# Optimization experiments

Hardware: AMD Instinct MI355X
Metric: run time of the kernel (lower is better)

## Reference

```python
import jax, jax.numpy as jnp
import numpy as np

B, D, H, E, C = 16384, 1024, 2048, 4, 3
EPS = 1e-5


def setup_inputs() -> dict:
    key = jax.random.key(0)
    ks = jax.random.split(key, 12)
    s = lambda k, shape, fan: jax.random.normal(k, shape, jnp.float32) * (1.0 / np.sqrt(fan))
    return {
        "x": jax.random.normal(ks[0], (B, D), jnp.float32),
        # gate: LayerNorm(D) -> Linear(D, E)
        "gate_ln_g": jnp.ones((D,), jnp.float32),
        "gate_ln_b": jnp.zeros((D,), jnp.float32),
        "gate_w": s(ks[1], (D, E), D),
        "gate_b": jnp.zeros((E,), jnp.float32),
        # experts (stacked over E): LayerNorm(D) -> Linear(D,H) -> GELU -> Linear(H,C)
        "ex_ln_g": jnp.ones((E, D), jnp.float32),
        "ex_ln_b": jnp.zeros((E, D), jnp.float32),
        "ex_w1": s(ks[2], (E, D, H), D),
        "ex_b1": jnp.zeros((E, H), jnp.float32),
        "ex_w2": s(ks[3], (E, H, C), H),
        "ex_b2": jnp.zeros((E, C), jnp.float32),
    }


def _normalize(x):
    # shared (x - mean) / sqrt(var + eps); per-expert affine applied separately
    mu = jnp.mean(x, axis=-1, keepdims=True)
    var = jnp.mean(jnp.square(x - mu), axis=-1, keepdims=True)
    return (x - mu) * jax.lax.rsqrt(var + EPS)


def reference(x, gate_ln_g, gate_ln_b, gate_w, gate_b,
              ex_ln_g, ex_ln_b, ex_w1, ex_b1, ex_w2, ex_b2):
    normed = _normalize(x)                              # [B, D]
    # gate: LN -> Linear -> softmax over experts
    gate_logits = (normed * gate_ln_g + gate_ln_b) @ gate_w + gate_b   # [B, E]
    gate_weights = jax.nn.softmax(gate_logits, axis=-1)               # [B, E]
    # experts (dropout inactive in eval): per-expert LN affine, MLP with exact GELU
    xn = normed[None, :, :] * ex_ln_g[:, None, :] + ex_ln_b[:, None, :]  # [E, B, D]
    h = jax.nn.gelu(jnp.einsum('ebd,edh->ebh', xn, ex_w1) + ex_b1[:, None, :],
                    approximate=False)                                   # [E, B, H]
    logits = jnp.einsum('ebh,ehc->ebc', h, ex_w2) + ex_b2[:, None, :]    # [E, B, C]
    # gated sum over experts
    return jnp.einsum('be,ebc->bc', gate_weights, logits)               # [B, C]
```

## Files before the change

kernel.cpp:

```cpp
#include <hip/hip_runtime.h>
#include <hip/hip_bf16.h>

typedef __bf16 bf16x8 __attribute__((ext_vector_type(8)));
typedef float  f32x4  __attribute__((ext_vector_type(4)));

__device__ __forceinline__ unsigned short f2bf(float f) {
    union { float f; unsigned int u; } v; v.f = f;
    unsigned int u = v.u;
    unsigned int r = (u + 0x7fffu + ((u >> 16) & 1u)) >> 16;
    return (unsigned short)r;
}

typedef const __attribute__((address_space(1))) unsigned int* gptr_t;
typedef __attribute__((address_space(3))) unsigned int* lptr_t;
__device__ __forceinline__ void async_ld16(const void* g, void* l) {
    __builtin_amdgcn_global_load_lds((gptr_t)g, (lptr_t)l, 16, 0, 0);
}

__device__ __forceinline__ float gelu_fast(float x) {
    const float c1 = 2.30223608f;
    const float c2 = 0.102944903f;
    float s  = x * x;
    float zn = x * __builtin_fmaf(s, -c2, -c1);
    float u  = __builtin_amdgcn_exp2f(zn);
    return x * __builtin_amdgcn_rcpf(1.0f + u);
}

#define Bn 16384
#define Dd 1024
#define Hh 2048
#define Ee 4
#define Cc 3

__global__ __launch_bounds__(256) void prep_and_norm(
        const float* __restrict__ x,
        const float* __restrict__ gg, const float* __restrict__ gb,
        const float* __restrict__ gw, const float* __restrict__ gbias,
        const float* __restrict__ w1, const float* __restrict__ exlng,
        const float* __restrict__ exlnb,
        unsigned short* __restrict__ normed, float* __restrict__ gate,
        unsigned short* __restrict__ w1t, float* __restrict__ b1part) {
    __shared__ float tile[64][65];
    __shared__ float red[4][64];
    const int bid = blockIdx.x, t = threadIdx.x;

    if (bid < 4096) {
        const int row  = bid * 4 + (t >> 6);
        const int lane = t & 63;
        const float4* xp = (const float4*)(x + (size_t)row * Dd);
        float4 v[4];
        float s = 0.f, q = 0.f;
        #pragma unroll
        for (int j = 0; j < 4; ++j) {
            v[j] = xp[j * 64 + lane];
            s += v[j].x + v[j].y + v[j].z + v[j].w;
            q += v[j].x * v[j].x + v[j].y * v[j].y + v[j].z * v[j].z + v[j].w * v[j].w;
        }
        #pragma unroll
        for (int off = 32; off; off >>= 1) { s += __shfl_xor(s, off); q += __shfl_xor(q, off); }
        const float mu = s * (1.f / Dd);
        const float var = q * (1.f / Dd) - mu * mu;
        const float rstd = rsqrtf(var + 1e-5f);
        float l0 = 0.f, l1 = 0.f, l2 = 0.f, l3 = 0.f;
        #pragma unroll
        for (int j = 0; j < 4; ++j) {
            const int d = j * 256 + lane * 4;
            float n[4] = { (v[j].x - mu) * rstd, (v[j].y - mu) * rstd,
                           (v[j].z - mu) * rstd, (v[j].w - mu) * rstd };
            ushort4 u; u.x = f2bf(n[0]); u.y = f2bf(n[1]); u.z = f2bf(n[2]); u.w = f2bf(n[3]);
            ((ushort4*)(normed + (size_t)row * Dd))[j * 64 + lane] = u;
            float4 g4 = ((const float4*)gg)[j * 64 + lane];
            float4 b4 = ((const float4*)gb)[j * 64 + lane];
            float a[4] = { n[0] * g4.x + b4.x, n[1] * g4.y + b4.y,
                           n[2] * g4.z + b4.z, n[3] * g4.w + b4.w };
            #pragma unroll
            for (int c = 0; c < 4; ++c) {
                float4 wv = ((const float4*)gw)[d + c];
                l0 += a[c] * wv.x; l1 += a[c] * wv.y; l2 += a[c] * wv.z; l3 += a[c] * wv.w;
            }
        }
        #pragma unroll
        for (int off = 32; off; off >>= 1) {
            l0 += __shfl_xor(l0, off); l1 += __shfl_xor(l1, off);
            l2 += __shfl_xor(l2, off); l3 += __shfl_xor(l3, off);
        }
        if (lane == 0) {
            float L0 = l0 + gbias[0], L1 = l1 + gbias[1], L2 = l2 + gbias[2], L3 = l3 + gbias[3];
            float mx = fmaxf(fmaxf(L0, L1), fmaxf(L2, L3));
            float e0 = expf(L0 - mx), e1 = expf(L1 - mx), e2 = expf(L2 - mx), e3 = expf(L3 - mx);
            float inv = 1.f / (e0 + e1 + e2 + e3);
            float4 gv; gv.x = e0 * inv; gv.y = e1 * inv; gv.z = e2 * inv; gv.w = e3 * inv;
            ((float4*)gate)[row] = gv;
        }
    } else {
        const int b2i = bid - 4096;
        const int d0b = b2i & 15, h0b = (b2i >> 4) & 31, e = b2i >> 9;
        const int d0 = d0b * 64, h0 = h0b * 64;
        const float* gp = exlng + e * Dd + d0;
        const float* lb = exlnb + e * Dd + d0;
        const float* wp = w1 + ((size_t)e * Dd + d0) * Hh + h0;
        #pragma unroll
        for (int j = 0; j < 16; ++j) {
            int idx = t + j * 256; int dl = idx >> 6, hl = idx & 63;
            tile[dl][hl] = wp[(size_t)dl * Hh + hl];
        }
        __syncthreads();
        #pragma unroll
        for (int j = 0; j < 8; ++j) {
            int idx = t + j * 256; int hl = idx >> 5, k2 = (idx & 31) * 2;
            ushort2 o; o.x = f2bf(tile[k2][hl] * gp[k2]); o.y = f2bf(tile[k2 + 1][hl] * gp[k2 + 1]);
            *(ushort2*)(w1t + ((size_t)(e * Hh + h0 + hl)) * Dd + d0 + k2) = o;
        }
        const int hl = t & 63, dq = t >> 6;
        float acc = 0.f;
        #pragma unroll
        for (int i = 0; i < 16; ++i)
            acc += lb[dq * 16 + i] * tile[dq * 16 + i][hl];
        red[dq][hl] = acc;
        __syncthreads();
        if (t < 64)
            b1part[(size_t)(e * 16 + d0b) * Hh + h0 + t] = red[0][t] + red[1][t] + red[2][t] + red[3][t];
    }
}

__global__ __launch_bounds__(512, 2) void gemm_fused(
    const unsigned short* __restrict__ A,
    const unsigned short* __restrict__ Bt,
    const float* __restrict__ b1,
    const float* __restrict__ b1part,
    const float* __restrict__ w2,
    float* __restrict__ part)
{
    __shared__ unsigned short As[4][256 * 32];
    __shared__ unsigned short Bs[4][256 * 32];
    __shared__ float w2s[256 * 3];
    __shared__ float b1s[256];

    const int L = blockIdx.x;
    const int xcd = L & 7, j = L >> 3;
    const int mb = (j >> 7) * 32 + xcd * 4 + (j & 3);
    const int nb = (j >> 2) & 31;
    const int m0 = mb * 256;
    const int n0 = nb * 256;

    const int t = threadIdx.x, lane = t & 63, wid = t >> 6;
    const int wm = wid >> 2, wn = wid & 3;
    const int quad = lane >> 4, l15 = lane & 15;

    if (t < 256) {
        const int e = n0 >> 11, hh = n0 & 2047;
        float s = b1[n0 + t];
        #pragma unroll
        for (int i = 0; i < 16; ++i)
            s += b1part[(size_t)(e * 16 + i) * Hh + hh + t];
        b1s[t] = s;
        w2s[t * 3 + 0] = w2[(n0 + t) * 3 + 0];
        w2s[t * 3 + 1] = w2[(n0 + t) * 3 + 1];
        w2s[t * 3 + 2] = w2[(n0 + t) * 3 + 2];
    }

    const int srow  = t >> 2;
    const int sslot = (t & 3) ^ ((t >> 3) & 3);
    const unsigned short* ga = A  + (size_t)(m0 + srow) * Dd + sslot * 8;
    const unsigned short* gb = Bt + (size_t)(n0 + srow) * Dd + sslot * 8;
    const int ldoff = t * 8;

#define STAGE_A(kt) { unsigned short* d = &As[(kt) & 3][ldoff];                 \
    async_ld16(ga + (kt) * 32,            d);                                   \
    async_ld16(ga + (kt) * 32 + 128 * Dd, d + 4096); }
#define STAGE_B(kt) { unsigned short* d = &Bs[(kt) & 3][ldoff];                 \
    async_ld16(gb + (kt) * 32,            d);                                   \
    async_ld16(gb + (kt) * 32 + 128 * Dd, d + 4096); }

    f32x4 acc[8][4] = {};

    const int rsw   = (l15 >> 1) & 3;
    const int aBase = (wm * 128 + l15) * 32 + ((quad ^ rsw) * 8);
    const int bBase = (wn * 64  + l15) * 32 + ((quad ^ rsw) * 8);

    STAGE_A(0); STAGE_B(0);
    STAGE_A(1); STAGE_B(1);
    __syncthreads();

    for (int kt = 0; kt < 32; ++kt) {
        const unsigned short* as = &As[kt & 3][0];
        const unsigned short* bs = &Bs[kt & 3][0];

        bf16x8 bf[4], af[8];
        #pragma unroll
        for (int ni = 0; ni < 4; ++ni) bf[ni] = *(const bf16x8*)(bs + bBase + ni * 512);
        #pragma unroll
        for (int mi = 0; mi < 8; ++mi) af[mi] = *(const bf16x8*)(as + aBase + mi * 512);

        if (kt < 30) { STAGE_A(kt + 2); STAGE_B(kt + 2); }

        if (kt < 30) {
            __asm__ volatile("s_waitcnt vmcnt(4)" ::: "memory");
        } else {
            __asm__ volatile("s_waitcnt vmcnt(0)" ::: "memory");
        }
        __builtin_amdgcn_s_barrier();
        __builtin_amdgcn_sched_barrier(0xF);

        __builtin_amdgcn_s_setprio(1);
        #pragma unroll
        for (int mi = 0; mi < 8; ++mi)
            #pragma unroll
            for (int ni = 0; ni < 4; ++ni)
                acc[mi][ni] = __builtin_amdgcn_mfma_f32_16x16x32_bf16(af[mi], bf[ni], acc[mi][ni], 0, 0, 0);
        __builtin_amdgcn_s_setprio(0);
    }
#undef STAGE_A
#undef STAGE_B

    __syncthreads();
    float* redb = (float*)&As[0][0];

    #pragma unroll
    for (int mi = 0; mi < 8; ++mi) {
        float pr[4][3];
        #pragma unroll
        for (int r = 0; r < 4; ++r) { pr[r][0] = 0.f; pr[r][1] = 0.f; pr[r][2] = 0.f; }
        #pragma unroll
        for (int ni = 0; ni < 4; ++ni) {
            const int nl = wn * 64 + ni * 16 + l15;
            const float b1v = b1s[nl];
            const float wa = w2s[nl * 3 + 0], wb = w2s[nl * 3 + 1], wc = w2s[nl * 3 + 2];
            #pragma unroll
            for (int r = 0; r < 4; ++r) {
                float xh = acc[mi][ni][r] + b1v;
                float h = gelu_fast(xh);
                pr[r][0] += h * wa; pr[r][1] += h * wb; pr[r][2] += h * wc;
            }
        }
        #pragma unroll
        for (int off = 1; off < 16; off <<= 1) {
            #pragma unroll
            for (int r = 0; r < 4; ++r) {
                pr[r][0] += __shfl_xor(pr[r][0], off);
                pr[r][1] += __shfl_xor(pr[r][1], off);
                pr[r][2] += __shfl_xor(pr[r][2], off);
            }
        }
        if (l15 == 0) {
            #pragma unroll
            for (int r = 0; r < 4; ++r) {
                const int rl = wm * 128 + mi * 16 + quad * 4 + r;
                float* rb = redb + (rl * 4 + wn) * 3;
                rb[0] = pr[r][0]; rb[1] = pr[r][1]; rb[2] = pr[r][2];
            }
        }
    }
    __syncthreads();
    if (t < 256) {
        const float* rb = redb + t * 12;
        float o0 = rb[0] + rb[3] + rb[6] + rb[9];
        float o1 = rb[1] + rb[4] + rb[7] + rb[10];
        float o2 = rb[2] + rb[5] + rb[8] + rb[11];
        float* pp = part + (size_t)(m0 + t) * 96 + nb * 3;
        pp[0] = o0; pp[1] = o1; pp[2] = o2;
    }
}

__global__ __launch_bounds__(256) void reduce_out(
        const float* __restrict__ part, const float* __restrict__ gate,
        const float* __restrict__ b2, float* __restrict__ out) {
    const int row = blockIdx.x * 256 + threadIdx.x;
    const float4 gv = ((const float4*)gate)[row];
    const float g[4] = { gv.x, gv.y, gv.z, gv.w };
    float o0 = g[0] * b2[0] + g[1] * b2[3] + g[2] * b2[6] + g[3] * b2[9];
    float o1 = g[0] * b2[1] + g[1] * b2[4] + g[2] * b2[7] + g[3] * b2[10];
    float o2 = g[0] * b2[2] + g[1] * b2[5] + g[2] * b2[8] + g[3] * b2[11];
    const float* pp = part + (size_t)row * 96;
    #pragma unroll
    for (int nb = 0; nb < 32; ++nb) {
        const float ge = g[nb >> 3];
        o0 += ge * pp[nb * 3 + 0];
        o1 += ge * pp[nb * 3 + 1];
        o2 += ge * pp[nb * 3 + 2];
    }
    out[row * 3 + 0] = o0; out[row * 3 + 1] = o1; out[row * 3 + 2] = o2;
}

extern "C" void kernel_launch(void* const* d_in, const int* in_sizes, int n_in,
                              void* d_out, int out_size, void* d_ws, size_t ws_size,
                              hipStream_t stream) {
    const float* x     = (const float*)d_in[0];
    const float* gg    = (const float*)d_in[1];
    const float* gb    = (const float*)d_in[2];
    const float* gw    = (const float*)d_in[3];
    const float* gbias = (const float*)d_in[4];
    const float* exlng = (const float*)d_in[5];
    const float* exlnb = (const float*)d_in[6];
    const float* w1    = (const float*)d_in[7];
    const float* b1    = (const float*)d_in[8];
    const float* w2    = (const float*)d_in[9];
    const float* b2    = (const float*)d_in[10];
    float* out = (float*)d_out;

    char* ws = (char*)d_ws;
    unsigned short* normed = (unsigned short*)ws;
    unsigned short* w1t    = (unsigned short*)(ws + 33554432);
    float* b1part = (float*)(ws + 33554432 + 16777216);
    float* gate   = (float*)(ws + 33554432 + 16777216 + 524288);
    float* part   = (float*)(ws + 33554432 + 16777216 + 524288 + 262144);

    prep_and_norm<<<6144, 256, 0, stream>>>(x, gg, gb, gw, gbias, w1, exlng, exlnb,
                                            normed, gate, w1t, b1part);
    gemm_fused<<<2048, 512, 0, stream>>>(normed, w1t, b1, b1part, w2, part);
    reduce_out<<<64, 256, 0, stream>>>(part, gate, b2, out);
}
```

Baseline: 473.5 us.

## Shrink GEMM tile to 256x128 with triple buffering for higher occupancy

The fused GEMM tile shrinks from 256x256 to 256x128, and the per-wave accumulators drop from 8x4 to 4x4 MFMA tiles. LDS goes from 4 stages to 3 rotating stages with a smaller B buffer, and launch bounds now target 4 blocks per CU. The XCD-aware block swizzle is replaced by a plain 2D grid. This raises occupancy and latency hiding, at the cost of more A-matrix re-reads, a lower MFMA-to-load ratio, lost L2 locality from the swizzle, and a partial-sum buffer twice as wide for the reduce kernel.

```diff
diff --git a/kernel.cpp b/kernel.cpp
--- a/kernel.cpp
+++ b/kernel.cpp
@@ -123,7 +123,7 @@
     }
 }
 
-__global__ __launch_bounds__(512, 2) void gemm_fused(
+__global__ __launch_bounds__(512, 4) void gemm_fused(
     const unsigned short* __restrict__ A,
     const unsigned short* __restrict__ Bt,
     const float* __restrict__ b1,
@@ -131,23 +131,20 @@
     const float* __restrict__ w2,
     float* __restrict__ part)
 {
-    __shared__ unsigned short As[4][256 * 32];
-    __shared__ unsigned short Bs[4][256 * 32];
-    __shared__ float w2s[256 * 3];
-    __shared__ float b1s[256];
-
-    const int L = blockIdx.x;
-    const int xcd = L & 7, j = L >> 3;
-    const int mb = (j >> 7) * 32 + xcd * 4 + (j & 3);
-    const int nb = (j >> 2) & 31;
-    const int m0 = mb * 256;
-    const int n0 = nb * 256;
+    __shared__ unsigned short As[3][256 * 32];
+    __shared__ unsigned short Bs[3][128 * 32];
+    __shared__ float w2s[128 * 3];
+    __shared__ float b1s[128];
+
+    const int nb = blockIdx.x;
+    const int n0 = nb * 128;
+    const int m0 = blockIdx.y * 256;
 
     const int t = threadIdx.x, lane = t & 63, wid = t >> 6;
-    const int wm = wid >> 2, wn = wid & 3;
+    const int wm = wid >> 1, wn = wid & 1;
     const int quad = lane >> 4, l15 = lane & 15;
 
-    if (t < 256) {
+    if (t < 128) {
         const int e = n0 >> 11, hh = n0 & 2047;
         float s = b1[n0 + t];
         #pragma unroll
@@ -159,43 +156,42 @@
         w2s[t * 3 + 2] = w2[(n0 + t) * 3 + 2];
     }
 
-    const int srow  = t >> 2;
     const int sslot = (t & 3) ^ ((t >> 3) & 3);
-    const unsigned short* ga = A  + (size_t)(m0 + srow) * Dd + sslot * 8;
-    const unsigned short* gb = Bt + (size_t)(n0 + srow) * Dd + sslot * 8;
+    const unsigned short* ga = A  + (size_t)(m0 + (t >> 2)) * Dd + sslot * 8;
+    const unsigned short* gb = Bt + (size_t)(n0 + (t >> 2)) * Dd + sslot * 8;
     const int ldoff = t * 8;
 
-#define STAGE_A(kt) { unsigned short* d = &As[(kt) & 3][ldoff];                 \
+#define STAGE_A(kt, bufi) { unsigned short* d = &As[bufi][ldoff];               \
     async_ld16(ga + (kt) * 32,            d);                                   \
     async_ld16(ga + (kt) * 32 + 128 * Dd, d + 4096); }
-#define STAGE_B(kt) { unsigned short* d = &Bs[(kt) & 3][ldoff];                 \
-    async_ld16(gb + (kt) * 32,            d);                                   \
-    async_ld16(gb + (kt) * 32 + 128 * Dd, d + 4096); }
-
-    f32x4 acc[8][4] = {};
+#define STAGE_B(kt, bufi) { async_ld16(gb + (kt) * 32, &Bs[bufi][ldoff]); }
+
+    f32x4 acc[4][4] = {};
 
     const int rsw   = (l15 >> 1) & 3;
-    const int aBase = (wm * 128 + l15) * 32 + ((quad ^ rsw) * 8);
-    const int bBase = (wn * 64  + l15) * 32 + ((quad ^ rsw) * 8);
-
-    STAGE_A(0); STAGE_B(0);
-    STAGE_A(1); STAGE_B(1);
+    const int aBase = (wm * 64 + l15) * 32 + ((quad ^ rsw) * 8);
+    const int bBase = (wn * 64 + l15) * 32 + ((quad ^ rsw) * 8);
+
+    STAGE_A(0, 0); STAGE_B(0, 0);
+    STAGE_A(1, 1); STAGE_B(1, 1);
     __syncthreads();
 
+    int rd = 0;
     for (int kt = 0; kt < 32; ++kt) {
-        const unsigned short* as = &As[kt & 3][0];
-        const unsigned short* bs = &Bs[kt & 3][0];
-
-        bf16x8 bf[4], af[8];
+        const unsigned short* as = &As[rd][0];
+        const unsigned short* bs = &Bs[rd][0];
+        const int wrb = (rd + 2 >= 3) ? rd - 1 : rd + 2;
+
+        bf16x8 bf[4], af[4];
         #pragma unroll
         for (int ni = 0; ni < 4; ++ni) bf[ni] = *(const bf16x8*)(bs + bBase + ni * 512);
         #pragma unroll
-        for (int mi = 0; mi < 8; ++mi) af[mi] = *(const bf16x8*)(as + aBase + mi * 512);
-
-        if (kt < 30) { STAGE_A(kt + 2); STAGE_B(kt + 2); }
+        for (int mi = 0; mi < 4; ++mi) af[mi] = *(const bf16x8*)(as + aBase + mi * 512);
+
+        if (kt < 30) { STAGE_A(kt + 2, wrb); STAGE_B(kt + 2, wrb); }
 
         if (kt < 30) {
-            __asm__ volatile("s_waitcnt vmcnt(4)" ::: "memory");
+            __asm__ volatile("s_waitcnt vmcnt(3)" ::: "memory");
         } else {
             __asm__ volatile("s_waitcnt vmcnt(0)" ::: "memory");
         }
@@ -204,11 +200,13 @@
 
         __builtin_amdgcn_s_setprio(1);
         #pragma unroll
-        for (int mi = 0; mi < 8; ++mi)
+        for (int mi = 0; mi < 4; ++mi)
             #pragma unroll
             for (int ni = 0; ni < 4; ++ni)
                 acc[mi][ni] = __builtin_amdgcn_mfma_f32_16x16x32_bf16(af[mi], bf[ni], acc[mi][ni], 0, 0, 0);
         __builtin_amdgcn_s_setprio(0);
+
+        rd = (rd + 1 >= 3) ? 0 : rd + 1;
     }
 #undef STAGE_A
 #undef STAGE_B
@@ -217,7 +215,7 @@
     float* redb = (float*)&As[0][0];
 
     #pragma unroll
-    for (int mi = 0; mi < 8; ++mi) {
+    for (int mi = 0; mi < 4; ++mi) {
         float pr[4][3];
         #pragma unroll
         for (int r = 0; r < 4; ++r) { pr[r][0] = 0.f; pr[r][1] = 0.f; pr[r][2] = 0.f; }
@@ -245,19 +243,19 @@
         if (l15 == 0) {
             #pragma unroll
             for (int r = 0; r < 4; ++r) {
-                const int rl = wm * 128 + mi * 16 + quad * 4 + r;
-                float* rb = redb + (rl * 4 + wn) * 3;
+                const int rl = wm * 64 + mi * 16 + quad * 4 + r;
+                float* rb = redb + (rl * 2 + wn) * 3;
                 rb[0] = pr[r][0]; rb[1] = pr[r][1]; rb[2] = pr[r][2];
             }
         }
     }
     __syncthreads();
     if (t < 256) {
-        const float* rb = redb + t * 12;
-        float o0 = rb[0] + rb[3] + rb[6] + rb[9];
-        float o1 = rb[1] + rb[4] + rb[7] + rb[10];
-        float o2 = rb[2] + rb[5] + rb[8] + rb[11];
-        float* pp = part + (size_t)(m0 + t) * 96 + nb * 3;
+        const float* rb = redb + t * 6;
+        float o0 = rb[0] + rb[3];
+        float o1 = rb[1] + rb[4];
+        float o2 = rb[2] + rb[5];
+        float* pp = part + (size_t)(m0 + t) * 192 + nb * 3;
         pp[0] = o0; pp[1] = o1; pp[2] = o2;
     }
 }
@@ -271,10 +269,10 @@
     float o0 = g[0] * b2[0] + g[1] * b2[3] + g[2] * b2[6] + g[3] * b2[9];
     float o1 = g[0] * b2[1] + g[1] * b2[4] + g[2] * b2[7] + g[3] * b2[10];
     float o2 = g[0] * b2[2] + g[1] * b2[5] + g[2] * b2[8] + g[3] * b2[11];
-    const float* pp = part + (size_t)row * 96;
+    const float* pp = part + (size_t)row * 192;
     #pragma unroll
-    for (int nb = 0; nb < 32; ++nb) {
-        const float ge = g[nb >> 3];
+    for (int nb = 0; nb < 64; ++nb) {
+        const float ge = g[nb >> 4];
         o0 += ge * pp[nb * 3 + 0];
         o1 += ge * pp[nb * 3 + 1];
         o2 += ge * pp[nb * 3 + 2];
@@ -307,6 +305,6 @@
 
     prep_and_norm<<<6144, 256, 0, stream>>>(x, gg, gb, gw, gbias, w1, exlng, exlnb,
                                             normed, gate, w1t, b1part);
-    gemm_fused<<<2048, 512, 0, stream>>>(normed, w1t, b1, b1part, w2, part);
+    gemm_fused<<<dim3(64, 64), 512, 0, stream>>>(normed, w1t, b1, b1part, w2, part);
     reduce_out<<<64, 256, 0, stream>>>(part, gate, b2, out);
 }
```

Result: no change. 470.7 us (-0.6%).

## Deepen GEMM pipeline with register double-buffered LDS fragments and simple grid mapping

Applied to the files above, without the earlier changes.

Restructures the main GEMM K-loop so LDS fragment loads for the next k-tile interleave with MFMAs of the current one. It uses ping-pong B registers, prefetches 3 stages ahead instead of 2, and needs only one barrier per iteration. It also replaces the XCD-aware swizzled block mapping with a plain 2D grid. The intent is to hide LDS latency behind matrix math. The costs are higher register pressure and possibly worse L2 locality across XCDs from the simpler mapping.

```diff
diff --git a/kernel.cpp b/kernel.cpp
--- a/kernel.cpp
+++ b/kernel.cpp
@@ -136,11 +136,8 @@
     __shared__ float w2s[256 * 3];
     __shared__ float b1s[256];
 
-    const int L = blockIdx.x;
-    const int xcd = L & 7, j = L >> 3;
-    const int mb = (j >> 7) * 32 + xcd * 4 + (j & 3);
-    const int nb = (j >> 2) & 31;
-    const int m0 = mb * 256;
+    const int m0 = blockIdx.x * 256;
+    const int nb = blockIdx.y;
     const int n0 = nb * 256;
 
     const int t = threadIdx.x, lane = t & 63, wid = t >> 6;
@@ -159,10 +156,9 @@
         w2s[t * 3 + 2] = w2[(n0 + t) * 3 + 2];
     }
 
-    const int srow  = t >> 2;
     const int sslot = (t & 3) ^ ((t >> 3) & 3);
-    const unsigned short* ga = A  + (size_t)(m0 + srow) * Dd + sslot * 8;
-    const unsigned short* gb = Bt + (size_t)(n0 + srow) * Dd + sslot * 8;
+    const unsigned short* ga = A  + (size_t)(m0 + (t >> 2)) * Dd + sslot * 8;
+    const unsigned short* gb = Bt + (size_t)(n0 + (t >> 2)) * Dd + sslot * 8;
     const int ldoff = t * 8;
 
 #define STAGE_A(kt) { unsigned short* d = &As[(kt) & 3][ldoff];                 \
@@ -173,6 +169,7 @@
     async_ld16(gb + (kt) * 32 + 128 * Dd, d + 4096); }
 
     f32x4 acc[8][4] = {};
+    bf16x8 af[8], bfX[4], bfY[4];
 
     const int rsw   = (l15 >> 1) & 3;
     const int aBase = (wm * 128 + l15) * 32 + ((quad ^ rsw) * 8);
@@ -180,36 +177,55 @@
 
     STAGE_A(0); STAGE_B(0);
     STAGE_A(1); STAGE_B(1);
+    STAGE_A(2); STAGE_B(2);
+    __asm__ volatile("s_waitcnt vmcnt(4)" ::: "memory");
     __syncthreads();
-
-    for (int kt = 0; kt < 32; ++kt) {
-        const unsigned short* as = &As[kt & 3][0];
-        const unsigned short* bs = &Bs[kt & 3][0];
-
-        bf16x8 bf[4], af[8];
-        #pragma unroll
-        for (int ni = 0; ni < 4; ++ni) bf[ni] = *(const bf16x8*)(bs + bBase + ni * 512);
-        #pragma unroll
-        for (int mi = 0; mi < 8; ++mi) af[mi] = *(const bf16x8*)(as + aBase + mi * 512);
-
-        if (kt < 30) { STAGE_A(kt + 2); STAGE_B(kt + 2); }
-
-        if (kt < 30) {
-            __asm__ volatile("s_waitcnt vmcnt(4)" ::: "memory");
-        } else {
-            __asm__ volatile("s_waitcnt vmcnt(0)" ::: "memory");
-        }
-        __builtin_amdgcn_s_barrier();
-        __builtin_amdgcn_sched_barrier(0xF);
-
-        __builtin_amdgcn_s_setprio(1);
-        #pragma unroll
-        for (int mi = 0; mi < 8; ++mi)
-            #pragma unroll
-            for (int ni = 0; ni < 4; ++ni)
-                acc[mi][ni] = __builtin_amdgcn_mfma_f32_16x16x32_bf16(af[mi], bf[ni], acc[mi][ni], 0, 0, 0);
-        __builtin_amdgcn_s_setprio(0);
-    }
+    #pragma unroll
+    for (int ni = 0; ni < 4; ++ni) bfX[ni] = *(const bf16x8*)(&Bs[0][bBase + ni * 512]);
+    #pragma unroll
+    for (int mi = 0; mi < 8; ++mi) af[mi] = *(const bf16x8*)(&As[0][aBase + mi * 512]);
+
+#define KBODY(KT, BFC, BFN, DOSTAGE, DOPREF, WAIT4)                              \
+  {                                                                              \
+    const unsigned short* asn = &As[((KT) + 1) & 3][0];                          \
+    const unsigned short* bsn = &Bs[((KT) + 1) & 3][0];                          \
+    if (DOPREF) {                                                                \
+      _Pragma("unroll")                                                          \
+      for (int ni = 0; ni < 4; ++ni)                                             \
+        BFN[ni] = *(const bf16x8*)(bsn + bBase + ni * 512);                      \
+    }                                                                            \
+    if (DOSTAGE) { STAGE_A((KT) + 3); STAGE_B((KT) + 3); }                       \
+    __builtin_amdgcn_s_setprio(1);                                               \
+    _Pragma("unroll")                                                            \
+    for (int mi = 0; mi < 8; ++mi) {                                             \
+      _Pragma("unroll")                                                          \
+      for (int ni = 0; ni < 4; ++ni)                                             \
+        acc[mi][ni] = __builtin_amdgcn_mfma_f32_16x16x32_bf16(af[mi], BFC[ni],   \
+                                                              acc[mi][ni], 0, 0, 0); \
+      if (DOPREF) af[mi] = *(const bf16x8*)(asn + aBase + mi * 512);             \
+    }                                                                            \
+    __builtin_amdgcn_s_setprio(0);                                               \
+    if (WAIT4) { __asm__ volatile("s_waitcnt vmcnt(4)" ::: "memory"); }          \
+    else       { __asm__ volatile("s_waitcnt vmcnt(0)" ::: "memory"); }          \
+    __builtin_amdgcn_s_barrier();                                                \
+    __builtin_amdgcn_sched_barrier(0xF);                                         \
+  }
+
+    for (int kt = 0; kt < 28; kt += 2) {
+        KBODY(kt,     bfX, bfY, true, true, true);
+        KBODY(kt + 1, bfY, bfX, true, true, true);
+    }
+    KBODY(28, bfX, bfY, true,  true, true);
+    KBODY(29, bfY, bfX, false, true, false);
+    KBODY(30, bfX, bfY, false, true, false);
+    __builtin_amdgcn_s_setprio(1);
+    #pragma unroll
+    for (int mi = 0; mi < 8; ++mi)
+        #pragma unroll
+        for (int ni = 0; ni < 4; ++ni)
+            acc[mi][ni] = __builtin_amdgcn_mfma_f32_16x16x32_bf16(af[mi], bfY[ni], acc[mi][ni], 0, 0, 0);
+    __builtin_amdgcn_s_setprio(0);
+#undef KBODY
 #undef STAGE_A
 #undef STAGE_B
 
@@ -307,6 +323,6 @@
 
     prep_and_norm<<<6144, 256, 0, stream>>>(x, gg, gb, gw, gbias, w1, exlng, exlnb,
                                             normed, gate, w1t, b1part);
-    gemm_fused<<<2048, 512, 0, stream>>>(normed, w1t, b1, b1part, w2, part);
+    gemm_fused<<<dim3(64, 32), 512, 0, stream>>>(normed, w1t, b1, b1part, w2, part);
     reduce_out<<<64, 256, 0, stream>>>(part, gate, b2, out);
 }
```

Result: slower. 484.5 us (+2.3%).
